# Optimization experiments

Measured on AMD Instinct MI355X. Metric: run time of the kernel, lower is better.

Reference implementation:

```python
import jax, jax.numpy as jnp
import numpy as np

MAX_DIST = 8
GUIDANCE_WEIGHT = 0.4
EPS_MAG = 1e-6
EPS_COS = 1e-8
EPS_WSUM = 1e-8


def setup_inputs() -> dict:
    key = jax.random.key(0)
    k1, k2 = jax.random.split(key)
    embeddings = jax.random.normal(k1, (4, 2048, 1024), dtype=jnp.float32)
    guidance_trajectories = jax.random.normal(k2, (512, 1024), dtype=jnp.float32)
    return {"embeddings": embeddings, "guidance_trajectories": guidance_trajectories}


def reference(embeddings, guidance_trajectories):
    B, S, D = embeddings.shape
    W = min(MAX_DIST, S - 1)  # fixed max window size

    # consecutive-token trajectory vectors: diffs[t] = emb[t+1] - emb[t]
    diffs = embeddings[:, 1:, :] - embeddings[:, :-1, :]          # [B, S-1, D]

    # sliding windows of the last W diffs ending at pos-1
    pos = jnp.arange(S)[:, None]                                  # [S, 1]
    k = jnp.arange(W)[None, :]                                    # [1, W]
    idx = pos - W + k                                             # diff index per slot
    valid = (idx >= 0) & (pos >= 1)                               # [S, W]
    windows = diffs[:, jnp.clip(idx, 0, S - 2), :]                # [B, S, W, D]

    # torch.linspace(0.1, 1.0, w) weights, per-position window size w = min(pos, W);
    # valid entries occupy the last w slots of the W-wide window.
    w = jnp.minimum(pos, W)                                       # [S, 1]
    j = k - (W - w)                                               # local index within window
    lin = jnp.where(w > 1, 0.1 + 0.9 * j / jnp.maximum(w - 1, 1), 0.1)
    pos_weights = jnp.where(valid, lin, 0.0).astype(embeddings.dtype)  # [S, W]

    # normalize trajectory vectors, zero where magnitude <= 1e-6
    mag = jnp.linalg.norm(windows, axis=-1, keepdims=True)        # [B, S, W, 1]
    is_valid_mag = mag > EPS_MAG
    normed = jnp.where(is_valid_mag, windows / jnp.where(is_valid_mag, mag, 1.0), 0.0)

    mag_weights = jnp.tanh(mag * 2.0)                             # [B, S, W, 1]
    combined = pos_weights[None, :, :, None] * mag_weights        # [B, S, W, 1]

    # guidance influence: softmax over cosine similarity to guidance bank
    g_norm = jnp.linalg.norm(guidance_trajectories, axis=-1)      # [G]
    a_norm = jnp.linalg.norm(normed, axis=-1)                     # [B, S, W]
    dots = jnp.einsum('bswd,gd->bswg', normed, guidance_trajectories)
    sims = dots / (jnp.maximum(a_norm, EPS_COS)[..., None] * jnp.maximum(g_norm, EPS_COS))
    g_weights = jax.nn.softmax(sims * 2.0, axis=-1)               # [B, S, W, G]
    influence = jnp.einsum('bswg,gd->bswd', g_weights, guidance_trajectories)
    blended = (1.0 - GUIDANCE_WEIGHT) * normed + GUIDANCE_WEIGHT * influence

    weight_sum = jnp.maximum(combined.sum(axis=2), EPS_WSUM)      # [B, S, 1]
    trajectories = (blended * combined).sum(axis=2) / weight_sum  # [B, S, D]
    return trajectories
```

## Files before the change

kernel.cpp:

```cpp
#include <hip/hip_runtime.h>
#include <math.h>

#define B_ 4
#define S_ 2048
#define D_ 1024
#define G_ 512
#define T_ 2047
#define R_ 8188
#define RPAD 8192
#define MT 32
#define ABST 520

typedef __attribute__((ext_vector_type(8))) short short8;
typedef __attribute__((ext_vector_type(4))) short s16x4;
typedef __attribute__((ext_vector_type(4))) float f32x4;

#define WSOFF_RG2  0u
#define WSOFF_MAGW 2048u
#define WSOFF_BP1  34816u
#define WSOFF_BP2  1083392u
#define WSOFF_NH   2131968u
#define WSOFF_IH   18909184u

__device__ inline short to_bf16(float f) {
    union { float f; unsigned u; } v; v.f = f;
    unsigned r = v.u + 0x7fffu + ((v.u >> 16) & 1u);
    return (short)(r >> 16);
}
__device__ inline float fb(unsigned short h) {
    union { unsigned u; float f; } v;
    v.u = ((unsigned)h) << 16;
    return v.f;
}

__global__ __launch_bounds__(64) void prep1_kernel(const float* __restrict__ guid,
                                                   float* __restrict__ rg2,
                                                   short8* __restrict__ Bp1) {
    int g = blockIdx.x, lane = threadIdx.x;
    const float4* gp = (const float4*)(guid + (size_t)g * D_);
    float ss = 0.f;
#pragma unroll
    for (int i = 0; i < 4; ++i) {
        float4 v = gp[lane + 64 * i];
        ss += v.x * v.x + v.y * v.y + v.z * v.z + v.w * v.w;
    }
#pragma unroll
    for (int m = 32; m >= 1; m >>= 1) ss += __shfl_xor(ss, m, 64);
    if (lane == 0) rg2[g] = 2.0f / fmaxf(sqrtf(ss), 1e-8f);
#pragma unroll
    for (int h = 0; h < 2; ++h) {
        int kg = lane + 64 * h;
        const float* src = guid + (size_t)g * D_ + kg * 8;
        short8 v;
#pragma unroll
        for (int j = 0; j < 8; ++j) v[j] = to_bf16(src[j]);
        Bp1[(size_t)kg * G_ + g] = v;
    }
}

__global__ __launch_bounds__(256) void prep2_kernel(const float* __restrict__ guid,
                                                    short8* __restrict__ Bp2) {
    int gg = blockIdx.x, tid = threadIdx.x;
#pragma unroll
    for (int dd = 0; dd < 4; ++dd) {
        int d = tid + 256 * dd;
        short8 v;
#pragma unroll
        for (int j = 0; j < 8; ++j) v[j] = to_bf16(guid[(size_t)(gg * 8 + j) * D_ + d]);
        Bp2[(size_t)gg * D_ + d] = v;
    }
}

__global__ __launch_bounds__(1024, 4) void fused_kernel(const float* __restrict__ emb,
                                                        const short8* __restrict__ Bp1,
                                                        const short8* __restrict__ Bp2,
                                                        const float* __restrict__ rg2,
                                                        float* __restrict__ magw,
                                                        short* __restrict__ normh,
                                                        short* __restrict__ inflh) {
    __shared__ short AB[MT][ABST];
    __shared__ float rg2s[G_];
    __shared__ float pred[MT][16];
    __shared__ float redmx[MT], redrs[MT];

    const int tid = threadIdx.x;
    const int wave = tid >> 6, lane = tid & 63;
    const int l15 = lane & 15, quad = lane >> 4;
    const int r0 = blockIdx.x * MT;

    if (tid < G_) rg2s[tid] = rg2[tid];

    s16x4 hold[2][2];
#pragma unroll
    for (int i = 0; i < 2; ++i) {
        int rr = wave * 2 + i;
        int R = r0 + rr;
        if (R < R_) {
            int b = R / T_;
            int t = R - b * T_;
            const float4* p = (const float4*)(emb + ((size_t)b * S_ + t) * D_);
            float4 dv[4]; float ss = 0.f;
#pragma unroll
            for (int j = 0; j < 4; ++j) {
                float4 x0 = p[lane + 64 * j];
                float4 x1 = p[lane + 64 * j + 256];
                dv[j] = make_float4(x1.x - x0.x, x1.y - x0.y, x1.z - x0.z, x1.w - x0.w);
                ss += dv[j].x * dv[j].x + dv[j].y * dv[j].y + dv[j].z * dv[j].z + dv[j].w * dv[j].w;
            }
#pragma unroll
            for (int m = 32; m >= 1; m >>= 1) ss += __shfl_xor(ss, m, 64);
            float mag = sqrtf(ss);
            float rmag = (mag > 1e-6f) ? (1.0f / mag) : 0.0f;
            if (lane == 0) magw[R] = tanhf(2.0f * mag);
            s16x4 h[4];
#pragma unroll
            for (int j = 0; j < 4; ++j) {
                h[j][0] = to_bf16(dv[j].x * rmag); h[j][1] = to_bf16(dv[j].y * rmag);
                h[j][2] = to_bf16(dv[j].z * rmag); h[j][3] = to_bf16(dv[j].w * rmag);
            }
            short* nb = normh + (size_t)R * D_ + 4 * lane;
#pragma unroll
            for (int j = 0; j < 4; ++j) *(s16x4*)(nb + 256 * j) = h[j];
            *(s16x4*)&AB[rr][4 * lane] = h[0];
            *(s16x4*)&AB[rr][4 * lane + 256] = h[1];
            hold[i][0] = h[2]; hold[i][1] = h[3];
        } else {
            s16x4 z = (s16x4)0;
            *(s16x4*)&AB[rr][4 * lane] = z;
            *(s16x4*)&AB[rr][4 * lane + 256] = z;
            hold[i][0] = z; hold[i][1] = z;
        }
    }
    __syncthreads();

    f32x4 acc1[2][2];
#pragma unroll
    for (int mt = 0; mt < 2; ++mt)
#pragma unroll
        for (int nt = 0; nt < 2; ++nt) acc1[mt][nt] = (f32x4)0.f;
#pragma unroll
    for (int p = 0; p < 2; ++p) {
        if (p == 1) {
            __syncthreads();
#pragma unroll
            for (int i = 0; i < 2; ++i) {
                int rr = wave * 2 + i;
                *(s16x4*)&AB[rr][4 * lane] = hold[i][0];
                *(s16x4*)&AB[rr][4 * lane + 256] = hold[i][1];
            }
            __syncthreads();
        }
        const short8* Bb = Bp1 + ((size_t)(64 * p + quad)) * G_ + wave * 32 + l15;
        short8 bc0 = Bb[0], bc1 = Bb[16], bn0, bn1;
        for (int ks = 0; ks < 16; ++ks) {
            if (ks < 15) {
                const short8* Bx = Bb + (size_t)(ks + 1) * 4 * G_;
                bn0 = Bx[0]; bn1 = Bx[16];
            }
            short8 a0 = *(const short8*)&AB[l15][ks * 32 + quad * 8];
            short8 a1 = *(const short8*)&AB[16 + l15][ks * 32 + quad * 8];
            acc1[0][0] = __builtin_amdgcn_mfma_f32_16x16x32_bf16(a0, bc0, acc1[0][0], 0, 0, 0);
            acc1[0][1] = __builtin_amdgcn_mfma_f32_16x16x32_bf16(a0, bc1, acc1[0][1], 0, 0, 0);
            acc1[1][0] = __builtin_amdgcn_mfma_f32_16x16x32_bf16(a1, bc0, acc1[1][0], 0, 0, 0);
            acc1[1][1] = __builtin_amdgcn_mfma_f32_16x16x32_bf16(a1, bc1, acc1[1][1], 0, 0, 0);
            bc0 = bn0; bc1 = bn1;
        }
    }

    {
        float pmax[2][4];
#pragma unroll
        for (int mt = 0; mt < 2; ++mt)
#pragma unroll
            for (int r2 = 0; r2 < 4; ++r2) pmax[mt][r2] = -1e30f;
#pragma unroll
        for (int mt = 0; mt < 2; ++mt)
#pragma unroll
            for (int nt = 0; nt < 2; ++nt) {
                float rgv = rg2s[wave * 32 + nt * 16 + l15];
#pragma unroll
                for (int r2 = 0; r2 < 4; ++r2) {
                    float lg = acc1[mt][nt][r2] * rgv;
                    acc1[mt][nt][r2] = lg;
                    pmax[mt][r2] = fmaxf(pmax[mt][r2], lg);
                }
            }
#pragma unroll
        for (int m = 8; m >= 1; m >>= 1)
#pragma unroll
            for (int mt = 0; mt < 2; ++mt)
#pragma unroll
                for (int r2 = 0; r2 < 4; ++r2)
                    pmax[mt][r2] = fmaxf(pmax[mt][r2], __shfl_xor(pmax[mt][r2], m, 16));
        if (l15 == 0) {
#pragma unroll
            for (int mt = 0; mt < 2; ++mt)
#pragma unroll
                for (int r2 = 0; r2 < 4; ++r2)
                    pred[mt * 16 + quad * 4 + r2][wave] = pmax[mt][r2];
        }
        __syncthreads();
        if (tid < MT) {
            float m = pred[tid][0];
#pragma unroll
            for (int w2 = 1; w2 < 16; ++w2) m = fmaxf(m, pred[tid][w2]);
            redmx[tid] = m;
        }
        __syncthreads();
        float psum[2][4];
#pragma unroll
        for (int mt = 0; mt < 2; ++mt)
#pragma unroll
            for (int r2 = 0; r2 < 4; ++r2) psum[mt][r2] = 0.f;
#pragma unroll
        for (int mt = 0; mt < 2; ++mt)
#pragma unroll
            for (int nt = 0; nt < 2; ++nt)
#pragma unroll
                for (int r2 = 0; r2 < 4; ++r2) {
                    float e = __expf(acc1[mt][nt][r2] - redmx[mt * 16 + quad * 4 + r2]);
                    acc1[mt][nt][r2] = e;
                    psum[mt][r2] += e;
                }
#pragma unroll
        for (int m = 8; m >= 1; m >>= 1)
#pragma unroll
            for (int mt = 0; mt < 2; ++mt)
#pragma unroll
                for (int r2 = 0; r2 < 4; ++r2)
                    psum[mt][r2] += __shfl_xor(psum[mt][r2], m, 16);
        if (l15 == 0) {
#pragma unroll
            for (int mt = 0; mt < 2; ++mt)
#pragma unroll
                for (int r2 = 0; r2 < 4; ++r2)
                    pred[mt * 16 + quad * 4 + r2][wave] = psum[mt][r2];
        }
        __syncthreads();
        if (tid < MT) {
            float s = 0.f;
#pragma unroll
            for (int w2 = 0; w2 < 16; ++w2) s += pred[tid][w2];
            redrs[tid] = 1.0f / s;
        }
        __syncthreads();
#pragma unroll
        for (int mt = 0; mt < 2; ++mt)
#pragma unroll
            for (int nt = 0; nt < 2; ++nt)
#pragma unroll
                for (int r2 = 0; r2 < 4; ++r2) {
                    int row = mt * 16 + quad * 4 + r2;
                    AB[row][wave * 32 + nt * 16 + l15] =
                        to_bf16(acc1[mt][nt][r2] * redrs[row]);
                }
    }
    __syncthreads();

    f32x4 acc2[2][4];
#pragma unroll
    for (int mt = 0; mt < 2; ++mt)
#pragma unroll
        for (int nt = 0; nt < 4; ++nt) acc2[mt][nt] = (f32x4)0.f;
    {
        const short8* Bb = Bp2 + (size_t)quad * D_ + wave * 64 + l15;
        short8 bc[4], bn[4];
#pragma unroll
        for (int nt = 0; nt < 4; ++nt) bc[nt] = Bb[nt * 16];
        for (int ks = 0; ks < 16; ++ks) {
            if (ks < 15) {
                const short8* Bx = Bb + (size_t)(ks + 1) * 4 * D_;
#pragma unroll
                for (int nt = 0; nt < 4; ++nt) bn[nt] = Bx[nt * 16];
            }
            short8 a0 = *(const short8*)&AB[l15][ks * 32 + quad * 8];
            short8 a1 = *(const short8*)&AB[16 + l15][ks * 32 + quad * 8];
#pragma unroll
            for (int nt = 0; nt < 4; ++nt) {
                acc2[0][nt] = __builtin_amdgcn_mfma_f32_16x16x32_bf16(a0, bc[nt], acc2[0][nt], 0, 0, 0);
                acc2[1][nt] = __builtin_amdgcn_mfma_f32_16x16x32_bf16(a1, bc[nt], acc2[1][nt], 0, 0, 0);
            }
#pragma unroll
            for (int nt = 0; nt < 4; ++nt) bc[nt] = bn[nt];
        }
    }

#pragma unroll
    for (int mt = 0; mt < 2; ++mt)
#pragma unroll
        for (int nt = 0; nt < 4; ++nt) {
            int d = wave * 64 + nt * 16 + l15;
#pragma unroll
            for (int r2 = 0; r2 < 4; ++r2) {
                int R = r0 + mt * 16 + quad * 4 + r2;
                if (R < R_) inflh[(size_t)R * D_ + d] = to_bf16(acc2[mt][nt][r2]);
            }
        }
}

__global__ __launch_bounds__(256) void combine_kernel(const float* __restrict__ magw,
                                                      const unsigned short* __restrict__ normh,
                                                      const unsigned short* __restrict__ inflh,
                                                      float* __restrict__ out) {
    int blk = blockIdx.x;
    int b = blk >> 8;
    int rem = blk & 255;
    int s0 = (rem >> 1) * 16;
    int d = (rem & 1) * 512 + threadIdx.x * 2;
    size_t rbase = (size_t)b * T_;

    float2 ring[8]; float mring[8];
#pragma unroll
    for (int a2 = 0; a2 < 8; ++a2) { ring[a2] = make_float2(0.f, 0.f); mring[a2] = 0.f; }

#define LOADBL(t_, dst_)                                                        \
    {                                                                           \
        size_t off_ = (rbase + (t_)) * D_ + d;                                  \
        ushort2 n2_ = *(const ushort2*)(normh + off_);                          \
        ushort2 i2_ = *(const ushort2*)(inflh + off_);                          \
        dst_ = make_float2(0.6f * fb(n2_.x) + 0.4f * fb(i2_.x),                 \
                           0.6f * fb(n2_.y) + 0.4f * fb(i2_.y));                \
    }

#pragma unroll
    for (int a2 = 0; a2 < 7; ++a2) {
        int t = s0 - 8 + a2;
        if (t >= 0) {
            LOADBL(t, ring[a2]);
            mring[a2] = magw[rbase + t];
        }
    }
    if (s0 != 0) {
#pragma unroll
        for (int i = 0; i < 16; ++i) {
            int t = s0 + i - 1;
            LOADBL(t, ring[(i + 7) & 7]);
            mring[(i + 7) & 7] = magw[rbase + t];
            float2 acc = make_float2(0.f, 0.f); float wsum = 0.f;
#pragma unroll
            for (int a = 1; a <= 8; ++a) {
                int slot = (i - a) & 7;
                float lin = 0.1f + (0.9f / 7.0f) * (float)(8 - a);
                float wt = lin * mring[slot];
                acc.x += wt * ring[slot].x; acc.y += wt * ring[slot].y;
                wsum += wt;
            }
            float rws = 1.0f / fmaxf(wsum, 1e-8f);
            *(float2*)&out[((size_t)b * S_ + s0 + i) * D_ + d] =
                make_float2(acc.x * rws, acc.y * rws);
        }
    } else {
#pragma unroll
        for (int i = 0; i < 16; ++i) {
            if (i >= 1) {
                int t = i - 1;
                LOADBL(t, ring[(i + 7) & 7]);
                mring[(i + 7) & 7] = magw[rbase + t];
            }
            int w = (i < 8) ? i : 8;
            float rw = (w > 1) ? 0.9f / (float)(w - 1) : 0.0f;
            float2 acc = make_float2(0.f, 0.f); float wsum = 0.f;
            for (int a = 1; a <= w; ++a) {
                int slot = (i - a) & 7;
                float lin = 0.1f + rw * (float)(w - a);
                float wt = lin * mring[slot];
                acc.x += wt * ring[slot].x; acc.y += wt * ring[slot].y;
                wsum += wt;
            }
            float rws = 1.0f / fmaxf(wsum, 1e-8f);
            *(float2*)&out[((size_t)b * S_ + i) * D_ + d] =
                make_float2(acc.x * rws, acc.y * rws);
        }
    }
#undef LOADBL
}

extern "C" void kernel_launch(void* const* d_in, const int* in_sizes, int n_in,
                              void* d_out, int out_size, void* d_ws, size_t ws_size,
                              hipStream_t stream) {
    const float* emb  = (const float*)d_in[0];
    const float* guid = (const float*)d_in[1];
    float* out = (float*)d_out;
    char* ws = (char*)d_ws;

    float*  rg2   = (float*)(ws + WSOFF_RG2);
    float*  magw  = (float*)(ws + WSOFF_MAGW);
    short8* Bp1   = (short8*)(ws + WSOFF_BP1);
    short8* Bp2   = (short8*)(ws + WSOFF_BP2);
    short*  normh = (short*)(ws + WSOFF_NH);
    short*  inflh = (short*)(ws + WSOFF_IH);

    prep1_kernel<<<G_, 64, 0, stream>>>(guid, rg2, Bp1);
    prep2_kernel<<<G_ / 8, 256, 0, stream>>>(guid, Bp2);
    fused_kernel<<<RPAD / MT, 1024, 0, stream>>>(emb, Bp1, Bp2, rg2, magw, normh, inflh);
    combine_kernel<<<B_ * 128 * 2, 256, 0, stream>>>(magw, (const unsigned short*)normh,
                                                     (const unsigned short*)inflh, out);
}
```

Measured before the change: 128.3 us.

## Merge prep kernels, deepen B prefetch, and restructure combine to per-row blocks

Fuses the two guidance preprocessing kernels into a single launch. In both MFMA GEMM phases, B operands are prefetched two k-steps ahead via a double buffer, and the second GEMM is split into two 32-column passes to reduce live accumulators. The combine kernel now assigns one block per output row with float4 accesses and a swizzled block order, dropping the register ring. This raises global re-reads of the bf16 intermediates, which the swizzle is meant to keep in L2.

```diff
diff --git a/kernel.cpp b/kernel.cpp
--- a/kernel.cpp
+++ b/kernel.cpp
@@ -33,37 +33,37 @@
     return v.f;
 }
 
-__global__ __launch_bounds__(64) void prep1_kernel(const float* __restrict__ guid,
+__global__ __launch_bounds__(256) void prep_kernel(const float* __restrict__ guid,
                                                    float* __restrict__ rg2,
-                                                   short8* __restrict__ Bp1) {
-    int g = blockIdx.x, lane = threadIdx.x;
-    const float4* gp = (const float4*)(guid + (size_t)g * D_);
-    float ss = 0.f;
-#pragma unroll
-    for (int i = 0; i < 4; ++i) {
-        float4 v = gp[lane + 64 * i];
-        ss += v.x * v.x + v.y * v.y + v.z * v.z + v.w * v.w;
-    }
-#pragma unroll
-    for (int m = 32; m >= 1; m >>= 1) ss += __shfl_xor(ss, m, 64);
-    if (lane == 0) rg2[g] = 2.0f / fmaxf(sqrtf(ss), 1e-8f);
-#pragma unroll
-    for (int h = 0; h < 2; ++h) {
-        int kg = lane + 64 * h;
-        const float* src = guid + (size_t)g * D_ + kg * 8;
-        short8 v;
-#pragma unroll
-        for (int j = 0; j < 8; ++j) v[j] = to_bf16(src[j]);
-        Bp1[(size_t)kg * G_ + g] = v;
-    }
-}
-
-__global__ __launch_bounds__(256) void prep2_kernel(const float* __restrict__ guid,
-                                                    short8* __restrict__ Bp2) {
-    int gg = blockIdx.x, tid = threadIdx.x;
-#pragma unroll
-    for (int dd = 0; dd < 4; ++dd) {
-        int d = tid + 256 * dd;
+                                                   short8* __restrict__ Bp1,
+                                                   short8* __restrict__ Bp2) {
+    int blk = blockIdx.x, tid = threadIdx.x;
+    if (blk < 128) {
+        int g = blk * 4 + (tid >> 6);
+        int lane = tid & 63;
+        const float4* gp = (const float4*)(guid + (size_t)g * D_);
+        float ss = 0.f;
+#pragma unroll
+        for (int i = 0; i < 4; ++i) {
+            float4 v = gp[lane + 64 * i];
+            ss += v.x * v.x + v.y * v.y + v.z * v.z + v.w * v.w;
+        }
+#pragma unroll
+        for (int m = 32; m >= 1; m >>= 1) ss += __shfl_xor(ss, m, 64);
+        if (lane == 0) rg2[g] = 2.0f / fmaxf(sqrtf(ss), 1e-8f);
+#pragma unroll
+        for (int h = 0; h < 2; ++h) {
+            int kg = lane + 64 * h;
+            const float* src = guid + (size_t)g * D_ + kg * 8;
+            short8 v;
+#pragma unroll
+            for (int j = 0; j < 8; ++j) v[j] = to_bf16(src[j]);
+            Bp1[(size_t)kg * G_ + g] = v;
+        }
+    } else {
+        int idx = blk - 128;
+        int gg = idx >> 2;
+        int d = (idx & 3) * 256 + tid;
         short8 v;
 #pragma unroll
         for (int j = 0; j < 8; ++j) v[j] = to_bf16(guid[(size_t)(gg * 8 + j) * D_ + d]);
@@ -151,19 +151,22 @@
             __syncthreads();
         }
         const short8* Bb = Bp1 + ((size_t)(64 * p + quad)) * G_ + wave * 32 + l15;
-        short8 bc0 = Bb[0], bc1 = Bb[16], bn0, bn1;
+        short8 buf[2][2];
+        buf[0][0] = Bb[0];             buf[0][1] = Bb[16];
+        buf[1][0] = Bb[4 * G_];        buf[1][1] = Bb[4 * G_ + 16];
+#pragma unroll
         for (int ks = 0; ks < 16; ++ks) {
-            if (ks < 15) {
-                const short8* Bx = Bb + (size_t)(ks + 1) * 4 * G_;
-                bn0 = Bx[0]; bn1 = Bx[16];
+            short8 b0 = buf[ks & 1][0], b1 = buf[ks & 1][1];
+            if (ks < 14) {
+                const short8* Bx = Bb + (size_t)(ks + 2) * 4 * G_;
+                buf[ks & 1][0] = Bx[0]; buf[ks & 1][1] = Bx[16];
             }
             short8 a0 = *(const short8*)&AB[l15][ks * 32 + quad * 8];
             short8 a1 = *(const short8*)&AB[16 + l15][ks * 32 + quad * 8];
-            acc1[0][0] = __builtin_amdgcn_mfma_f32_16x16x32_bf16(a0, bc0, acc1[0][0], 0, 0, 0);
-            acc1[0][1] = __builtin_amdgcn_mfma_f32_16x16x32_bf16(a0, bc1, acc1[0][1], 0, 0, 0);
-            acc1[1][0] = __builtin_amdgcn_mfma_f32_16x16x32_bf16(a1, bc0, acc1[1][0], 0, 0, 0);
-            acc1[1][1] = __builtin_amdgcn_mfma_f32_16x16x32_bf16(a1, bc1, acc1[1][1], 0, 0, 0);
-            bc0 = bn0; bc1 = bn1;
+            acc1[0][0] = __builtin_amdgcn_mfma_f32_16x16x32_bf16(a0, b0, acc1[0][0], 0, 0, 0);
+            acc1[0][1] = __builtin_amdgcn_mfma_f32_16x16x32_bf16(a0, b1, acc1[0][1], 0, 0, 0);
+            acc1[1][0] = __builtin_amdgcn_mfma_f32_16x16x32_bf16(a1, b0, acc1[1][0], 0, 0, 0);
+            acc1[1][1] = __builtin_amdgcn_mfma_f32_16x16x32_bf16(a1, b1, acc1[1][1], 0, 0, 0);
         }
     }
 
@@ -257,122 +260,86 @@
     }
     __syncthreads();
 
-    f32x4 acc2[2][4];
-#pragma unroll
-    for (int mt = 0; mt < 2; ++mt)
-#pragma unroll
-        for (int nt = 0; nt < 4; ++nt) acc2[mt][nt] = (f32x4)0.f;
-    {
-        const short8* Bb = Bp2 + (size_t)quad * D_ + wave * 64 + l15;
-        short8 bc[4], bn[4];
-#pragma unroll
-        for (int nt = 0; nt < 4; ++nt) bc[nt] = Bb[nt * 16];
+#pragma unroll
+    for (int dp = 0; dp < 2; ++dp) {
+        int d0 = wave * 64 + dp * 32;
+        f32x4 acc2[2][2];
+#pragma unroll
+        for (int mt = 0; mt < 2; ++mt)
+#pragma unroll
+            for (int nt = 0; nt < 2; ++nt) acc2[mt][nt] = (f32x4)0.f;
+        const short8* Bb = Bp2 + (size_t)quad * D_ + d0 + l15;
+        short8 buf[2][2];
+        buf[0][0] = Bb[0];            buf[0][1] = Bb[16];
+        buf[1][0] = Bb[4 * D_];       buf[1][1] = Bb[4 * D_ + 16];
+#pragma unroll
         for (int ks = 0; ks < 16; ++ks) {
-            if (ks < 15) {
-                const short8* Bx = Bb + (size_t)(ks + 1) * 4 * D_;
-#pragma unroll
-                for (int nt = 0; nt < 4; ++nt) bn[nt] = Bx[nt * 16];
+            short8 b0 = buf[ks & 1][0], b1 = buf[ks & 1][1];
+            if (ks < 14) {
+                const short8* Bx = Bb + (size_t)(ks + 2) * 4 * D_;
+                buf[ks & 1][0] = Bx[0]; buf[ks & 1][1] = Bx[16];
             }
             short8 a0 = *(const short8*)&AB[l15][ks * 32 + quad * 8];
             short8 a1 = *(const short8*)&AB[16 + l15][ks * 32 + quad * 8];
-#pragma unroll
-            for (int nt = 0; nt < 4; ++nt) {
-                acc2[0][nt] = __builtin_amdgcn_mfma_f32_16x16x32_bf16(a0, bc[nt], acc2[0][nt], 0, 0, 0);
-                acc2[1][nt] = __builtin_amdgcn_mfma_f32_16x16x32_bf16(a1, bc[nt], acc2[1][nt], 0, 0, 0);
-            }
-#pragma unroll
-            for (int nt = 0; nt < 4; ++nt) bc[nt] = bn[nt];
-        }
-    }
-
-#pragma unroll
-    for (int mt = 0; mt < 2; ++mt)
-#pragma unroll
-        for (int nt = 0; nt < 4; ++nt) {
-            int d = wave * 64 + nt * 16 + l15;
-#pragma unroll
-            for (int r2 = 0; r2 < 4; ++r2) {
-                int R = r0 + mt * 16 + quad * 4 + r2;
-                if (R < R_) inflh[(size_t)R * D_ + d] = to_bf16(acc2[mt][nt][r2]);
-            }
-        }
+            acc2[0][0] = __builtin_amdgcn_mfma_f32_16x16x32_bf16(a0, b0, acc2[0][0], 0, 0, 0);
+            acc2[0][1] = __builtin_amdgcn_mfma_f32_16x16x32_bf16(a0, b1, acc2[0][1], 0, 0, 0);
+            acc2[1][0] = __builtin_amdgcn_mfma_f32_16x16x32_bf16(a1, b0, acc2[1][0], 0, 0, 0);
+            acc2[1][1] = __builtin_amdgcn_mfma_f32_16x16x32_bf16(a1, b1, acc2[1][1], 0, 0, 0);
+        }
+#pragma unroll
+        for (int mt = 0; mt < 2; ++mt)
+#pragma unroll
+            for (int nt = 0; nt < 2; ++nt) {
+                int d = d0 + nt * 16 + l15;
+#pragma unroll
+                for (int r2 = 0; r2 < 4; ++r2) {
+                    int R = r0 + mt * 16 + quad * 4 + r2;
+                    if (R < R_) inflh[(size_t)R * D_ + d] = to_bf16(acc2[mt][nt][r2]);
+                }
+            }
+    }
 }
 
 __global__ __launch_bounds__(256) void combine_kernel(const float* __restrict__ magw,
                                                       const unsigned short* __restrict__ normh,
                                                       const unsigned short* __restrict__ inflh,
                                                       float* __restrict__ out) {
-    int blk = blockIdx.x;
-    int b = blk >> 8;
-    int rem = blk & 255;
-    int s0 = (rem >> 1) * 16;
-    int d = (rem & 1) * 512 + threadIdx.x * 2;
+    int flat = blockIdx.x;
+    int virt = ((flat & 7) << 10) | (flat >> 3);
+    int b = virt >> 11;
+    int s = virt & (S_ - 1);
+    int tid = threadIdx.x;
     size_t rbase = (size_t)b * T_;
 
-    float2 ring[8]; float mring[8];
-#pragma unroll
-    for (int a2 = 0; a2 < 8; ++a2) { ring[a2] = make_float2(0.f, 0.f); mring[a2] = 0.f; }
-
-#define LOADBL(t_, dst_)                                                        \
-    {                                                                           \
-        size_t off_ = (rbase + (t_)) * D_ + d;                                  \
-        ushort2 n2_ = *(const ushort2*)(normh + off_);                          \
-        ushort2 i2_ = *(const ushort2*)(inflh + off_);                          \
-        dst_ = make_float2(0.6f * fb(n2_.x) + 0.4f * fb(i2_.x),                 \
-                           0.6f * fb(n2_.y) + 0.4f * fb(i2_.y));                \
-    }
-
-#pragma unroll
-    for (int a2 = 0; a2 < 7; ++a2) {
-        int t = s0 - 8 + a2;
-        if (t >= 0) {
-            LOADBL(t, ring[a2]);
-            mring[a2] = magw[rbase + t];
-        }
-    }
-    if (s0 != 0) {
-#pragma unroll
-        for (int i = 0; i < 16; ++i) {
-            int t = s0 + i - 1;
-            LOADBL(t, ring[(i + 7) & 7]);
-            mring[(i + 7) & 7] = magw[rbase + t];
-            float2 acc = make_float2(0.f, 0.f); float wsum = 0.f;
-#pragma unroll
-            for (int a = 1; a <= 8; ++a) {
-                int slot = (i - a) & 7;
-                float lin = 0.1f + (0.9f / 7.0f) * (float)(8 - a);
-                float wt = lin * mring[slot];
-                acc.x += wt * ring[slot].x; acc.y += wt * ring[slot].y;
-                wsum += wt;
-            }
-            float rws = 1.0f / fmaxf(wsum, 1e-8f);
-            *(float2*)&out[((size_t)b * S_ + s0 + i) * D_ + d] =
-                make_float2(acc.x * rws, acc.y * rws);
-        }
-    } else {
-#pragma unroll
-        for (int i = 0; i < 16; ++i) {
-            if (i >= 1) {
-                int t = i - 1;
-                LOADBL(t, ring[(i + 7) & 7]);
-                mring[(i + 7) & 7] = magw[rbase + t];
-            }
-            int w = (i < 8) ? i : 8;
-            float rw = (w > 1) ? 0.9f / (float)(w - 1) : 0.0f;
-            float2 acc = make_float2(0.f, 0.f); float wsum = 0.f;
-            for (int a = 1; a <= w; ++a) {
-                int slot = (i - a) & 7;
-                float lin = 0.1f + rw * (float)(w - a);
-                float wt = lin * mring[slot];
-                acc.x += wt * ring[slot].x; acc.y += wt * ring[slot].y;
-                wsum += wt;
-            }
-            float rws = 1.0f / fmaxf(wsum, 1e-8f);
-            *(float2*)&out[((size_t)b * S_ + i) * D_ + d] =
-                make_float2(acc.x * rws, acc.y * rws);
-        }
-    }
-#undef LOADBL
+    int w = (s < 8) ? s : 8;
+    float rw = (w > 1) ? 0.9f / (float)(w - 1) : 0.0f;
+    float wt[8];
+    float wsum = 0.f;
+#pragma unroll
+    for (int j = 0; j < 8; ++j) {
+        float v = 0.f;
+        if (j < w) v = (0.1f + rw * (float)j) * magw[rbase + s - w + j];
+        wt[j] = v;
+        wsum += v;
+    }
+    float rws = 1.0f / fmaxf(wsum, 1e-8f);
+
+    float4 acc = make_float4(0.f, 0.f, 0.f, 0.f);
+#pragma unroll
+    for (int j = 0; j < 8; ++j) {
+        if (j < w) {
+            size_t off = (rbase + (size_t)(s - w + j)) * D_ + tid * 4;
+            ushort4 n = *(const ushort4*)(normh + off);
+            ushort4 iv = *(const ushort4*)(inflh + off);
+            float c = wt[j];
+            acc.x += c * (0.6f * fb(n.x) + 0.4f * fb(iv.x));
+            acc.y += c * (0.6f * fb(n.y) + 0.4f * fb(iv.y));
+            acc.z += c * (0.6f * fb(n.z) + 0.4f * fb(iv.z));
+            acc.w += c * (0.6f * fb(n.w) + 0.4f * fb(iv.w));
+        }
+    }
+    *(float4*)&out[((size_t)b * S_ + s) * D_ + tid * 4] =
+        make_float4(acc.x * rws, acc.y * rws, acc.z * rws, acc.w * rws);
 }
 
 extern "C" void kernel_launch(void* const* d_in, const int* in_sizes, int n_in,
@@ -390,9 +357,8 @@
     short*  normh = (short*)(ws + WSOFF_NH);
     short*  inflh = (short*)(ws + WSOFF_IH);
 
-    prep1_kernel<<<G_, 64, 0, stream>>>(guid, rg2, Bp1);
-    prep2_kernel<<<G_ / 8, 256, 0, stream>>>(guid, Bp2);
+    prep_kernel<<<384, 256, 0, stream>>>(guid, rg2, Bp1, Bp2);
     fused_kernel<<<RPAD / MT, 1024, 0, stream>>>(emb, Bp1, Bp2, rg2, magw, normh, inflh);
-    combine_kernel<<<B_ * 128 * 2, 256, 0, stream>>>(magw, (const unsigned short*)normh,
-                                                     (const unsigned short*)inflh, out);
-}
+    combine_kernel<<<B_ * S_, 256, 0, stream>>>(magw, (const unsigned short*)normh,
+                                                (const unsigned short*)inflh, out);
+}
```

Result: slower. 148.2 us (+15.5%).
